# Kernel tuning notes

Hardware: AMD Instinct MI355X
Metric: run time of the kernel (lower is better)

## Reference

```python
import jax, jax.numpy as jnp
import numpy as np

N, E, D, H = 100000, 1250000, 64, 128
EPS = 1e-5


def sage_bn_relu(x, src, dst, W_self, b_self, W_neigh, gamma, beta):
    # mean aggregation over in-neighbors (DGL SAGEConv 'mean')
    n = x.shape[0]
    deg = jax.ops.segment_sum(jnp.ones((src.shape[0],), x.dtype), dst, num_segments=n)
    agg = jax.ops.segment_sum(x[src], dst, num_segments=n)  # [N, d]
    neigh = agg / jnp.maximum(deg, 1.0)[:, None]             # zero in-degree -> 0
    h = x @ W_self + b_self + neigh @ W_neigh                # fc_self + fc_neigh
    # BatchNorm1d (training-mode batch statistics, biased variance)
    mu = h.mean(0)
    var = jnp.mean((h - mu) ** 2, axis=0)
    h = (h - mu) * jax.lax.rsqrt(var + EPS) * gamma + beta
    return jax.nn.relu(h)  # dropout omitted (deterministic eval)


def setup_inputs() -> dict:
    key = jax.random.key(0)
    ks = jax.random.split(key, 32)
    inp = {
        "x": jax.random.normal(ks[0], (N, D), jnp.float32),
        "src": jax.random.randint(ks[1], (E,), 0, N),
        "dst": jax.random.randint(ks[2], (E,), 0, N),
    }
    dims = [(D, H), (H, H), (H, H)]
    k = 3
    for i, (din, dout) in enumerate(dims):
        s = 1.0 / np.sqrt(din)
        inp[f"W_self{i}"] = jax.random.uniform(ks[k], (din, dout), jnp.float32, -s, s); k += 1
        inp[f"b_self{i}"] = jnp.zeros((dout,), jnp.float32)
        inp[f"W_neigh{i}"] = jax.random.uniform(ks[k], (din, dout), jnp.float32, -s, s); k += 1
        inp[f"gamma{i}"] = jnp.ones((dout,), jnp.float32)
        inp[f"beta{i}"] = jnp.zeros((dout,), jnp.float32)
    s = 1.0 / np.sqrt(H)
    inp["Wc"] = jax.random.uniform(ks[k], (H, 2), jnp.float32, -s, s)
    inp["bc"] = jnp.zeros((2,), jnp.float32)
    return inp


def reference(x, src, dst,
              W_self0, b_self0, W_neigh0, gamma0, beta0,
              W_self1, b_self1, W_neigh1, gamma1, beta1,
              W_self2, b_self2, W_neigh2, gamma2, beta2,
              Wc, bc):
    h = sage_bn_relu(x, src, dst, W_self0, b_self0, W_neigh0, gamma0, beta0)
    h = sage_bn_relu(h, src, dst, W_self1, b_self1, W_neigh1, gamma1, beta1)
    h = sage_bn_relu(h, src, dst, W_self2, b_self2, W_neigh2, gamma2, beta2)
    return h @ Wc + bc  # [N, 2]
```

## Files before the change

kernel.cpp:

```cpp
#include <hip/hip_runtime.h>


#define N_NODES 100000
#define N_EDGES 1250000
#define NB 1563
#define BSZ 64
#define CAP 1024
#define BPART 256
#define INVN (1.0f / 100000.0f)

typedef short bf16x8 __attribute__((ext_vector_type(8)));
typedef float f32x4 __attribute__((ext_vector_type(4)));
typedef unsigned short u16x8 __attribute__((ext_vector_type(8)));
typedef unsigned short u16x4 __attribute__((ext_vector_type(4)));

__device__ __forceinline__ float bf2f(unsigned short u) {
  union { unsigned int i; float f; } c; c.i = ((unsigned int)u) << 16; return c.f;
}
__device__ __forceinline__ unsigned short f2bf(float f) {
  union { float f; unsigned int i; } c; c.f = f;
  unsigned int r = (c.i + 0x7FFFu + ((c.i >> 16) & 1u)) >> 16;
  return (unsigned short)r;
}
__device__ __forceinline__ void bn_st(const float* stats, const float* gam,
                                      const float* bet, int c, float& s, float& t) {
  float sum = stats[c] + stats[256 + c] + stats[512 + c] + stats[768 + c];
  float sq  = stats[128 + c] + stats[384 + c] + stats[640 + c] + stats[896 + c];
  float mu = sum * INVN;
  float var = sq * INVN - mu * mu;
  s = gam[c] * rsqrtf(var + 1e-5f);
  t = bet[c] - mu * s;
}
__device__ __forceinline__ void gload_lds16(const void* g, void* l) {
  __builtin_amdgcn_global_load_lds(
      (const __attribute__((address_space(1))) unsigned int*)g,
      (__attribute__((address_space(3))) unsigned int*)l, 16, 0, 0);
}

__global__ __launch_bounds__(256) void k_prep(
    const float* __restrict__ x, unsigned short* __restrict__ x16,
    const float* __restrict__ W0s, const float* __restrict__ W0n,
    const float* __restrict__ W1s, const float* __restrict__ W1n,
    const float* __restrict__ W2s, const float* __restrict__ W2n,
    unsigned short* __restrict__ wt, float* __restrict__ stats3,
    const int* __restrict__ dst, int* __restrict__ hist, int E) {
  __shared__ int hh[NB];
  int blk = blockIdx.x, t = threadIdx.x;
  if (blk < 6250) {
    int i = blk * 256 + t;
    float4 v = ((const float4*)x)[i];
    u16x4 o;
    o.x = f2bf(v.x); o.y = f2bf(v.y); o.z = f2bf(v.z); o.w = f2bf(v.w);
    ((u16x4*)x16)[i] = o;
  } else if (blk < 6570) {
    int i = (blk - 6250) * 256 + t;
    if (i < 16384) {
      const float* W = (i < 8192) ? W0s : W0n;
      unsigned short* o = wt + (i < 8192 ? 0 : 8192);
      int j = i & 8191;
      int c = j >> 6, k = j & 63;
      o[j] = f2bf(W[k * 128 + c]);
    } else {
      int j = i - 16384;
      int sel = j >> 14;
      j &= 16383;
      const float* W = (sel == 0) ? W1s : (sel == 1) ? W1n : (sel == 2) ? W2s : W2n;
      unsigned short* o = wt + 16384 + sel * 16384;
      int c = j >> 7, k = j & 127;
      o[j] = f2bf(W[k * 128 + c]);
    }
  } else if (blk == 6570) {
    for (int i = t; i < 3 * 1024; i += 256) stats3[i] = 0.f;
  } else {
    int hb = blk - 6571;
    int chunk = (E + BPART - 1) / BPART;
    int start = hb * chunk;
    int end = min(E, start + chunk);
    for (int b = t; b < NB; b += 256) hh[b] = 0;
    __syncthreads();
    for (int e = start + t; e < end; e += 256) atomicAdd(&hh[dst[e] >> 6], 1);
    __syncthreads();
    for (int b = t; b < NB; b += 256) hist[hb * NB + b] = hh[b];
  }
}

__global__ __launch_bounds__(256) void k_scan(const int* __restrict__ hist,
                                              int* __restrict__ base,
                                              int* __restrict__ gcursor) {
  int bb = blockIdx.x * 256 + threadIdx.x;
  if (bb >= NB) return;
  int run = 0;
  for (int r0 = 0; r0 < BPART; r0 += 16) {
    int v[16];
    #pragma unroll
    for (int u = 0; u < 16; u++) v[u] = hist[(r0 + u) * NB + bb];
    #pragma unroll
    for (int u = 0; u < 16; u++) { base[(r0 + u) * NB + bb] = run; run += v[u]; }
  }
  gcursor[bb] = run;
}

__global__ __launch_bounds__(256) void k_scatter(const int* __restrict__ src,
                                                 const int* __restrict__ dst,
                                                 const int* __restrict__ base,
                                                 unsigned int* __restrict__ part, int E) {
  __shared__ int cur[NB];
  int t = threadIdx.x;
  int chunk = (E + BPART - 1) / BPART;
  int start = blockIdx.x * chunk;
  int end = min(E, start + chunk);
  for (int b = t; b < NB; b += 256) cur[b] = base[blockIdx.x * NB + b];
  __syncthreads();
  for (int e = start + t; e < end; e += 256) {
    int d = dst[e];
    int b = d >> 6;
    int pos = atomicAdd(&cur[b], 1);
    if ((unsigned)pos < (unsigned)CAP)
      part[(size_t)b * CAP + pos] = (unsigned)src[e] | ((unsigned)(d & 63) << 17);
  }
}

template <int DIN, bool BN>
__global__ __launch_bounds__(512, 8) void k_layer(
    const unsigned short* __restrict__ h, const unsigned short* __restrict__ W1t,
    const unsigned short* __restrict__ W2t, const float* __restrict__ bias,
    const unsigned int* __restrict__ part, const int* __restrict__ gcursor,
    unsigned short* __restrict__ C, float* __restrict__ stats, int M,
    const float* __restrict__ statsP, const float* __restrict__ gamP,
    const float* __restrict__ betP) {
  __shared__ unsigned short neighT[64 * DIN];
  __shared__ unsigned eord[CAP];
  __shared__ unsigned short Bs[128 * 32];
  __shared__ int cnt[BSZ], offv[BSZ], cur[BSZ];
  __shared__ int stealCtr;
  __shared__ float sBN[128], tBN[128];
  unsigned* eraw = (unsigned*)neighT;
  float* redS = (float*)eord;
  float* redQ = redS + 512;

  constexpr int SWZM = (DIN == 128) ? 15 : 7;
  int t = threadIdx.x;
  int lane = t & 63, w = t >> 6;
  int l15 = lane & 15, quad = lane >> 4;
  int bkt = blockIdx.x;
  int node0 = bkt * BSZ;
  int nn = min(BSZ, M - node0);

  if (t < BSZ) cnt[t] = 0;
  if (t == 0) stealCtr = 0;
  if (BN && t < 128) bn_st(statsP, gamP, betP, t, sBN[t], tBN[t]);
  __syncthreads();

  int ec = gcursor[bkt];
  ec = max(0, min(ec, CAP));
  for (int i = t; i < ec; i += 512) {
    unsigned wd = part[(size_t)bkt * CAP + i];
    eraw[i] = wd;
    atomicAdd(&cnt[wd >> 17], 1);
  }
  __syncthreads();
  if (t < BSZ) offv[t] = cnt[t];
  __syncthreads();
  #pragma unroll
  for (int o = 1; o < BSZ; o <<= 1) {
    int xv = 0;
    if (t < BSZ && t >= o) xv = offv[t - o];
    __syncthreads();
    if (t < BSZ) offv[t] += xv;
    __syncthreads();
  }
  if (t < BSZ) { int ex = offv[t] - cnt[t]; offv[t] = ex; cur[t] = ex; }
  __syncthreads();
  for (int i = t; i < ec; i += 512) {
    unsigned wd = eraw[i];
    int p = atomicAdd(&cur[wd >> 17], 1);
    eord[p] = wd & 0x1FFFF;
  }
  __syncthreads();

  const int G = DIN / 8;
  int li = t & (G - 1);
  float sreg[8], treg[8];
  if (BN) {
    #pragma unroll
    for (int k = 0; k < 8; k++) { sreg[k] = sBN[li * 8 + k]; treg[k] = tBN[li * 8 + k]; }
  }
  for (;;) {
    int nd0 = 0;
    if (li == 0) nd0 = atomicAdd(&stealCtr, 1);
    int nd = __shfl(nd0, 0, G);
    if (nd >= BSZ) break;
    u16x8 o;
    if (nd >= nn) {
      #pragma unroll
      for (int k = 0; k < 8; k++) o[k] = 0;
    } else {
      int s = offv[nd], c = cnt[nd];
      int e = s + c;
      float acc[8] = {0.f, 0.f, 0.f, 0.f, 0.f, 0.f, 0.f, 0.f};
      int j = s;
      for (; j + 2 <= e; j += 2) {
        int sn0 = eord[j], sn1 = eord[j + 1];
        u16x8 v0 = *(const u16x8*)&h[(size_t)sn0 * DIN + li * 8];
        u16x8 v1 = *(const u16x8*)&h[(size_t)sn1 * DIN + li * 8];
        if (BN) {
          #pragma unroll
          for (int k = 0; k < 8; k++)
            acc[k] += fmaxf(fmaf(bf2f(v0[k]), sreg[k], treg[k]), 0.f)
                    + fmaxf(fmaf(bf2f(v1[k]), sreg[k], treg[k]), 0.f);
        } else {
          #pragma unroll
          for (int k = 0; k < 8; k++) acc[k] += bf2f(v0[k]) + bf2f(v1[k]);
        }
      }
      if (j < e) {
        int sn = eord[j];
        u16x8 v = *(const u16x8*)&h[(size_t)sn * DIN + li * 8];
        if (BN) {
          #pragma unroll
          for (int k = 0; k < 8; k++)
            acc[k] += fmaxf(fmaf(bf2f(v[k]), sreg[k], treg[k]), 0.f);
        } else {
          #pragma unroll
          for (int k = 0; k < 8; k++) acc[k] += bf2f(v[k]);
        }
      }
      float inv = 1.0f / fmaxf((float)c, 1.0f);
      #pragma unroll
      for (int k = 0; k < 8; k++) o[k] = f2bf(acc[k] * inv);
    }
    *(u16x8*)&neighT[nd * DIN + ((li * 8) ^ ((nd & SWZM) << 3))] = o;
  }
  __syncthreads();

  const int strip = w >> 1;
  const int ch = w & 1;
  const int row = strip * 16 + l15;
  f32x4 acc4[4];
  #pragma unroll
  for (int ct = 0; ct < 4; ct++) acc4[ct] = (f32x4){0.f, 0.f, 0.f, 0.f};

  #pragma unroll
  for (int half = 0; half < 2; half++) {
    const unsigned short* Wt = half ? W2t : W1t;
    for (int k0 = 0; k0 < DIN; k0 += 32) {
      {
        int r = t >> 2, prt = t & 3;
        gload_lds16(&Wt[(size_t)r * DIN + k0 + prt * 8], &Bs[(w * 64) * 8]);
      }
      __syncthreads();
      bf16x8 af;
      {
        u16x8 v;
        if (half == 0) {
          v = *(const u16x8*)&h[(size_t)(node0 + row) * DIN + k0 + quad * 8];
          if (BN) {
            #pragma unroll
            for (int j = 0; j < 8; j++) {
              int c = k0 + quad * 8 + j;
              v[j] = f2bf(fmaxf(fmaf(bf2f(v[j]), sBN[c], tBN[c]), 0.f));
            }
          }
        } else {
          int cc = k0 + quad * 8;
          v = *(const u16x8*)&neighT[row * DIN + (cc ^ ((row & SWZM) << 3))];
        }
        af = *(bf16x8*)&v;
      }
      #pragma unroll
      for (int ct = 0; ct < 4; ct++) {
        bf16x8 bfr = *(const bf16x8*)&Bs[(ch * 64 + ct * 16 + l15) * 32 + quad * 8];
        acc4[ct] = __builtin_amdgcn_mfma_f32_16x16x32_bf16(af, bfr, acc4[ct], 0, 0, 0);
      }
      __syncthreads();
    }
  }

  float bcol[4], ls[4], lq[4];
  #pragma unroll
  for (int ct = 0; ct < 4; ct++) {
    bcol[ct] = bias[ch * 64 + ct * 16 + l15];
    ls[ct] = 0.f; lq[ct] = 0.f;
  }
  #pragma unroll
  for (int r = 0; r < 4; r++) {
    int orow = node0 + strip * 16 + quad * 4 + r;
    if (orow < M) {
      #pragma unroll
      for (int ct = 0; ct < 4; ct++) {
        float v = acc4[ct][r] + bcol[ct];
        C[(size_t)orow * 128 + ch * 64 + ct * 16 + l15] = f2bf(v);
        ls[ct] += v; lq[ct] += v * v;
      }
    }
  }
  #pragma unroll
  for (int ct = 0; ct < 4; ct++) {
    ls[ct] += __shfl_xor(ls[ct], 16); ls[ct] += __shfl_xor(ls[ct], 32);
    lq[ct] += __shfl_xor(lq[ct], 16); lq[ct] += __shfl_xor(lq[ct], 32);
  }
  if (quad == 0) {
    #pragma unroll
    for (int ct = 0; ct < 4; ct++) {
      redS[w * 64 + ct * 16 + l15] = ls[ct];
      redQ[w * 64 + ct * 16 + l15] = lq[ct];
    }
  }
  __syncthreads();
  if (t < 128) {
    int ch2 = t >> 6, c6 = t & 63;
    float s = 0.f, q = 0.f;
    #pragma unroll
    for (int st = 0; st < 4; st++) {
      s += redS[(st * 2 + ch2) * 64 + c6];
      q += redQ[(st * 2 + ch2) * 64 + c6];
    }
    int rep = (bkt & 3) * 256;
    atomicAdd(&stats[rep + t], s);
    atomicAdd(&stats[rep + 128 + t], q);
  }
}

__global__ void k_final(const unsigned short* __restrict__ h,
                        const float* __restrict__ statsP, const float* __restrict__ gamP,
                        const float* __restrict__ betP, const float* __restrict__ Wc,
                        const float* __restrict__ bc, float* __restrict__ out, int n) {
  int lane = threadIdx.x & 63;
  int row = blockIdx.x * (blockDim.x >> 6) + (threadIdx.x >> 6);
  if (row >= n) return;
  float acc0 = 0.f, acc1 = 0.f;
  #pragma unroll
  for (int m = 0; m < 2; m++) {
    int c = lane + 64 * m;
    float s, tt;
    bn_st(statsP, gamP, betP, c, s, tt);
    float v = bf2f(h[(size_t)row * 128 + c]);
    v = fmaxf(fmaf(v, s, tt), 0.f);
    acc0 += v * Wc[c * 2 + 0];
    acc1 += v * Wc[c * 2 + 1];
  }
  #pragma unroll
  for (int off = 32; off > 0; off >>= 1) {
    acc0 += __shfl_down(acc0, off);
    acc1 += __shfl_down(acc1, off);
  }
  if (lane == 0) {
    out[row * 2 + 0] = acc0 + bc[0];
    out[row * 2 + 1] = acc1 + bc[1];
  }
}

extern "C" void kernel_launch(void* const* d_in, const int* in_sizes, int n_in,
                              void* d_out, int out_size, void* d_ws, size_t ws_size,
                              hipStream_t stream) {
  const float* x   = (const float*)d_in[0];
  const int* src   = (const int*)d_in[1];
  const int* dst   = (const int*)d_in[2];
  const float* Wself[3] = {(const float*)d_in[3], (const float*)d_in[8],  (const float*)d_in[13]};
  const float* bself[3] = {(const float*)d_in[4], (const float*)d_in[9],  (const float*)d_in[14]};
  const float* Wngh[3]  = {(const float*)d_in[5], (const float*)d_in[10], (const float*)d_in[15]};
  const float* gam[3]   = {(const float*)d_in[6], (const float*)d_in[11], (const float*)d_in[16]};
  const float* bet[3]   = {(const float*)d_in[7], (const float*)d_in[12], (const float*)d_in[17]};
  const float* Wc = (const float*)d_in[18];
  const float* bc = (const float*)d_in[19];
  float* out = (float*)d_out;

  const int N = N_NODES, E = N_EDGES;

  unsigned short* x16 = (unsigned short*)d_ws;
  unsigned short* b0  = x16 + (size_t)N * 64;
  unsigned short* b1  = b0 + (size_t)N * 128;
  unsigned short* b2  = b1 + (size_t)N * 128;
  unsigned short* wt  = b2 + (size_t)N * 128;
  unsigned int* part  = (unsigned int*)(wt + 81920);
  int* gcursor  = (int*)(part + (size_t)NB * CAP);
  float* stats3 = (float*)(gcursor + NB);

  int* hist = (int*)b1;
  int* base = hist + (size_t)BPART * NB;

  k_prep<<<6571 + BPART, 256, 0, stream>>>(
      x, x16, Wself[0], Wngh[0], Wself[1], Wngh[1], Wself[2], Wngh[2],
      wt, stats3, dst, hist, E);

  k_scan<<<(NB + 255) / 256, 256, 0, stream>>>(hist, base, gcursor);
  k_scatter<<<BPART, 256, 0, stream>>>(src, dst, base, part, E);

  k_layer<64, false><<<NB, 512, 0, stream>>>(
      x16, wt + 0, wt + 8192, bself[0], part, gcursor, b1, stats3 + 0, N,
      nullptr, nullptr, nullptr);
  k_layer<128, true><<<NB, 512, 0, stream>>>(
      b1, wt + 16384, wt + 32768, bself[1], part, gcursor, b2, stats3 + 1024, N,
      stats3 + 0, gam[0], bet[0]);
  k_layer<128, true><<<NB, 512, 0, stream>>>(
      b2, wt + 49152, wt + 65536, bself[2], part, gcursor, b1, stats3 + 2048, N,
      stats3 + 1024, gam[1], bet[1]);

  k_final<<<(N + 3) / 4, 256, 0, stream>>>(b1, stats3 + 2048, gam[2], bet[2],
                                           Wc, bc, out, N);
}
```

Measured before the change: 375.9 us.

## Hoist self GEMM before aggregation and double-buffer swizzled neighbor weight tiles

The self-feature MFMA product (h @ W_self) is moved ahead of neighbor aggregation and reads W1t fragments straight from global memory, with no LDS staging or barriers. The neighbor GEMM now double-buffers its weight tile in LDS with an XOR swizzle, which cuts barriers per K-step and LDS bank conflicts. The goal is to overlap global latency with the gather phase and shorten the serialized GEMM tail. In exchange it uses more LDS and keeps the accumulators live across the gather loop, which adds register pressure. It also adds a barrier before the reduction, because redS aliases the eord buffer.

```diff
diff --git a/kernel.cpp b/kernel.cpp
--- a/kernel.cpp
+++ b/kernel.cpp
@@ -130,7 +130,7 @@
     const float* __restrict__ betP) {
   __shared__ unsigned short neighT[64 * DIN];
   __shared__ unsigned eord[CAP];
-  __shared__ unsigned short Bs[128 * 32];
+  __shared__ unsigned short Bs[2][128 * 32];
   __shared__ int cnt[BSZ], offv[BSZ], cur[BSZ];
   __shared__ int stealCtr;
   __shared__ float sBN[128], tBN[128];
@@ -139,6 +139,7 @@
   float* redQ = redS + 512;
 
   constexpr int SWZM = (DIN == 128) ? 15 : 7;
+  constexpr int KS = DIN / 32;
   int t = threadIdx.x;
   int lane = t & 63, w = t >> 6;
   int l15 = lane & 15, quad = lane >> 4;
@@ -177,6 +178,31 @@
     eord[p] = wd & 0x1FFFF;
   }
   __syncthreads();
+
+  const int strip = w >> 1;
+  const int ch = w & 1;
+  const int row = strip * 16 + l15;
+  f32x4 acc4[4];
+  #pragma unroll
+  for (int ct = 0; ct < 4; ct++) acc4[ct] = (f32x4){0.f, 0.f, 0.f, 0.f};
+  #pragma unroll
+  for (int s = 0; s < KS; s++) {
+    int k0 = s * 32;
+    u16x8 v = *(const u16x8*)&h[(size_t)(node0 + row) * DIN + k0 + quad * 8];
+    if (BN) {
+      #pragma unroll
+      for (int j = 0; j < 8; j++) {
+        int c = k0 + quad * 8 + j;
+        v[j] = f2bf(fmaxf(fmaf(bf2f(v[j]), sBN[c], tBN[c]), 0.f));
+      }
+    }
+    bf16x8 af = *(bf16x8*)&v;
+    #pragma unroll
+    for (int ct = 0; ct < 4; ct++) {
+      u16x8 bv = *(const u16x8*)&W1t[(size_t)(ch * 64 + ct * 16 + l15) * DIN + k0 + quad * 8];
+      acc4[ct] = __builtin_amdgcn_mfma_f32_16x16x32_bf16(af, *(bf16x8*)&bv, acc4[ct], 0, 0, 0);
+    }
+  }
 
   const int G = DIN / 8;
   int li = t & (G - 1);
@@ -231,49 +257,30 @@
     }
     *(u16x8*)&neighT[nd * DIN + ((li * 8) ^ ((nd & SWZM) << 3))] = o;
   }
-  __syncthreads();
-
-  const int strip = w >> 1;
-  const int ch = w & 1;
-  const int row = strip * 16 + l15;
-  f32x4 acc4[4];
-  #pragma unroll
-  for (int ct = 0; ct < 4; ct++) acc4[ct] = (f32x4){0.f, 0.f, 0.f, 0.f};
-
-  #pragma unroll
-  for (int half = 0; half < 2; half++) {
-    const unsigned short* Wt = half ? W2t : W1t;
-    for (int k0 = 0; k0 < DIN; k0 += 32) {
-      {
-        int r = t >> 2, prt = t & 3;
-        gload_lds16(&Wt[(size_t)r * DIN + k0 + prt * 8], &Bs[(w * 64) * 8]);
-      }
-      __syncthreads();
-      bf16x8 af;
-      {
-        u16x8 v;
-        if (half == 0) {
-          v = *(const u16x8*)&h[(size_t)(node0 + row) * DIN + k0 + quad * 8];
-          if (BN) {
-            #pragma unroll
-            for (int j = 0; j < 8; j++) {
-              int c = k0 + quad * 8 + j;
-              v[j] = f2bf(fmaxf(fmaf(bf2f(v[j]), sBN[c], tBN[c]), 0.f));
-            }
-          }
-        } else {
-          int cc = k0 + quad * 8;
-          v = *(const u16x8*)&neighT[row * DIN + (cc ^ ((row & SWZM) << 3))];
-        }
-        af = *(bf16x8*)&v;
-      }
-      #pragma unroll
-      for (int ct = 0; ct < 4; ct++) {
-        bf16x8 bfr = *(const bf16x8*)&Bs[(ch * 64 + ct * 16 + l15) * 32 + quad * 8];
-        acc4[ct] = __builtin_amdgcn_mfma_f32_16x16x32_bf16(af, bfr, acc4[ct], 0, 0, 0);
-      }
-      __syncthreads();
-    }
+
+  auto stageBs = [&](int k0, int bi) {
+    int r = t >> 2, c = t & 3;
+    int p = c ^ ((r >> 1) & 3);
+    gload_lds16(&W2t[(size_t)r * DIN + k0 + p * 8], &Bs[bi][(w * 64) * 8]);
+  };
+  stageBs(0, 0);
+  __syncthreads();
+
+  int cb = 0;
+  #pragma unroll
+  for (int s = 0; s < KS; s++) {
+    if (s + 1 < KS) stageBs((s + 1) * 32, cb ^ 1);
+    int cc = s * 32 + quad * 8;
+    u16x8 v = *(const u16x8*)&neighT[row * DIN + (cc ^ ((row & SWZM) << 3))];
+    bf16x8 af = *(bf16x8*)&v;
+    #pragma unroll
+    for (int ct = 0; ct < 4; ct++) {
+      int brow = ch * 64 + ct * 16 + l15;
+      bf16x8 bfr = *(const bf16x8*)&Bs[cb][brow * 32 + ((quad ^ ((brow >> 1) & 3)) * 8)];
+      acc4[ct] = __builtin_amdgcn_mfma_f32_16x16x32_bf16(af, bfr, acc4[ct], 0, 0, 0);
+    }
+    if (s + 1 < KS) __syncthreads();
+    cb ^= 1;
   }
 
   float bcol[4], ls[4], lq[4];
@@ -294,6 +301,7 @@
       }
     }
   }
+  __syncthreads();
   #pragma unroll
   for (int ct = 0; ct < 4; ct++) {
     ls[ct] += __shfl_xor(ls[ct], 16); ls[ct] += __shfl_xor(ls[ct], 32);
```

Result: slower. 410.0 us (+9.1%).
